# Performance work log

Measured on AMD Instinct MI355X. Metric: run time of the kernel, lower is better.

Reference implementation:

```python
import jax, jax.numpy as jnp
import numpy as np

B, S, V = 512, 256, 10      # batch, s_node_num, v_node_num
E, H = 128, 128             # embedding, lstm hidden
D = 2 * H                   # num_directions * hidden
PENALTY = 1.0e6
STD = 0.1


def _cell(x, h, c, Wih, Whh, b):
    # PyTorch LSTM cell, gate order i, f, g, o; b = b_ih + b_hh
    g = x @ Wih.T + h @ Whh.T + b
    i, f, gg, o = jnp.split(g, 4, axis=-1)
    c = jax.nn.sigmoid(f) * c + jax.nn.sigmoid(i) * jnp.tanh(gg)
    h = jax.nn.sigmoid(o) * jnp.tanh(c)
    return h, c


def setup_inputs() -> dict:
    key = jax.random.key(0)
    ks = jax.random.split(key, 25)
    w = lambda k, shp: (jax.random.normal(k, shp, jnp.float32) * STD)
    return {
        's_node_indexes': jax.random.randint(ks[0], (B, S), 0, S, dtype=jnp.int32),
        's_inputs': jax.random.uniform(ks[1], (B, S, 3), jnp.float32),
        'v_input': jax.random.uniform(ks[2], (V, 3), jnp.float32) * 0.5,
        'W_embed': w(ks[3], (E, 1)),
        'enc_Wih_f': w(ks[4], (4 * H, E)), 'enc_Whh_f': w(ks[5], (4 * H, H)), 'enc_b_f': w(ks[6], (4 * H,)),
        'enc_Wih_b': w(ks[7], (4 * H, E)), 'enc_Whh_b': w(ks[8], (4 * H, H)), 'enc_b_b': w(ks[9], (4 * H,)),
        'dec_Wih_f': w(ks[10], (4 * H, D)), 'dec_Whh_f': w(ks[11], (4 * H, H)), 'dec_b_f': w(ks[12], (4 * H,)),
        'dec_Wih_b': w(ks[13], (4 * H, D)), 'dec_Whh_b': w(ks[14], (4 * H, H)), 'dec_b_b': w(ks[15], (4 * H,)),
        'W_ref': w(ks[16], (D, D)), 'W_q': w(ks[17], (D, D)), 'v_w': w(ks[18], (D,)),
        'W_ref2': w(ks[19], (D, D)), 'W_q2': w(ks[20], (D, D)), 'v2_w': w(ks[21], (D,)),
    }


def reference(s_node_indexes, s_inputs, v_input, W_embed,
              enc_Wih_f, enc_Whh_f, enc_b_f, enc_Wih_b, enc_Whh_b, enc_b_b,
              dec_Wih_f, dec_Whh_f, dec_b_f, dec_Wih_b, dec_Whh_b, dec_b_b,
              W_ref, W_q, v_w, W_ref2, W_q2, v2_w):
    Bn, Sn = s_node_indexes.shape
    # Embed: snode resource -> Linear(1, E, bias=False)
    emb = s_inputs[:, :, 0:1] @ W_embed.T            # (B, S, E)
    xs = jnp.swapaxes(emb, 0, 1)                     # (S, B, E)
    h0 = jnp.zeros((Bn, H), jnp.float32)
    c0 = jnp.zeros((Bn, H), jnp.float32)

    def enc_scan(Wih, Whh, b, seq):
        def step(carry, x):
            h, c = carry
            h, c = _cell(x, h, c, Wih, Whh, b)
            return (h, c), h
        (hT, cT), hs = jax.lax.scan(step, (h0, c0), seq)
        return hs, hT, cT

    hs_f, hf, cf = enc_scan(enc_Wih_f, enc_Whh_f, enc_b_f, xs)
    hs_b, hb, cb = enc_scan(enc_Wih_b, enc_Whh_b, enc_b_b, xs[::-1])
    Enc = jnp.swapaxes(jnp.concatenate([hs_f, hs_b[::-1]], axis=-1), 0, 1)  # (B, S, D)
    h_state = jnp.stack([hf, hb])                    # (2, B, H)
    c_state = jnp.stack([cf, cb])

    refE = Enc @ W_ref.T                             # (B, S, D) precomputed (dropout p=0)
    ref2E = Enc @ W_ref2.T

    def dec_step(carry, vcpu):
        dec_in, h, c, played = carry                 # dec_in (B, D)
        hf_, cf_ = _cell(dec_in, h[0], c[0], dec_Wih_f, dec_Whh_f, dec_b_f)
        hb_, cb_ = _cell(dec_in, h[1], c[1], dec_Wih_b, dec_Whh_b, dec_b_b)
        dec_out = jnp.concatenate([hf_, hb_], axis=-1)                       # (B, D)
        cannot = (s_inputs[:, :, 0] < vcpu).astype(jnp.float32) + played     # (B, S)
        ow = jnp.tanh(refE + (dec_out @ W_q.T)[:, None, :]) @ v_w - PENALTY * cannot
        att = jax.nn.softmax(jnp.tanh(ref2E + (dec_in @ W_q2.T)[:, None, :]) @ v2_w, axis=1)
        new_in = jnp.einsum('bs,bsd->bd', att, Enc)
        sel = jnp.argmax(ow, axis=1)
        played = played + jax.nn.one_hot(sel, Sn, dtype=jnp.float32)
        return (new_in, jnp.stack([hf_, hb_]), jnp.stack([cf_, cb_]), played), (ow, sel)

    init = (jnp.zeros((Bn, D), jnp.float32), h_state, c_state, jnp.zeros((Bn, Sn), jnp.float32))
    _, (output_weights, sels) = jax.lax.scan(dec_step, init, v_input[:, 0])
    shuffled = sels.T                                # (B, V)
    original = jnp.take_along_axis(s_node_indexes, shuffled, axis=1)
    return original, shuffled, output_weights        # output_weights: (V, B, S)
```

## Files before the change

### kernel.cpp

```cpp
#include <hip/hip_runtime.h>
#include <math.h>

#define cB 512
#define cS 256
#define cV 10
#define cE 128
#define cH 128
#define cD 256
#define cG 512
#define PEN 1.0e6f
#define PADK 40
#define S1OW 112
#define L1OW 144
#define S2AT 128
#define L2AT 128

typedef _Float16 half8_t __attribute__((ext_vector_type(8)));
typedef _Float16 half4_t __attribute__((ext_vector_type(4)));
typedef float f32x4 __attribute__((ext_vector_type(4)));

#define DOT4(acc, wv, hv)                                   \
    do {                                                    \
        acc = fmaf((wv).x, (hv).x, acc);                    \
        acc = fmaf((wv).y, (hv).y, acc);                    \
        acc = fmaf((wv).z, (hv).z, acc);                    \
        acc = fmaf((wv).w, (hv).w, acc);                    \
    } while (0)

__device__ __forceinline__ float sigmf(float x) { return 1.0f / (1.0f + expf(-x)); }

__global__ void k_uprep(const float* __restrict__ Wih_f, const float* __restrict__ Wih_b,
                        const float* __restrict__ W_embed, float* __restrict__ uvec)
{
    const int j = threadIdx.x;
    const float* __restrict__ Wih = blockIdx.x ? Wih_b : Wih_f;
    float u = 0.f;
#pragma unroll 8
    for (int e = 0; e < cE; ++e) u = fmaf(Wih[(size_t)j * cE + e], W_embed[e], u);
    uvec[blockIdx.x * cG + j] = u;
}

__global__ __launch_bounds__(1024, 2) void k_encoder(
    const float* __restrict__ s_inputs, const float* __restrict__ uvec,
    const float* __restrict__ Whh_f, const float* __restrict__ b_f,
    const float* __restrict__ Whh_b, const float* __restrict__ b_b,
    _Float16* __restrict__ Ehi, _Float16* __restrict__ Elo,
    float* __restrict__ h_state, float* __restrict__ c_state)
{
    const int dir = blockIdx.x >> 7;
    const int b0  = (blockIdx.x & 127) * 4;
    const float* __restrict__ Whh = dir ? Whh_b : Whh_f;
    const float* __restrict__ bv  = dir ? b_b   : b_f;
    const int tid = threadIdx.x;
    const int jj = tid & 255;
    const int q  = tid >> 8;

    __shared__ __align__(16) float a_in[4][cS];
    __shared__ __align__(16) float hbuf[4][132];
    __shared__ __align__(16) float gpart[16][520];

    a_in[tid >> 8][tid & 255] =
        s_inputs[((size_t)(b0 + (tid >> 8)) * cS + (tid & 255)) * 3];

    float4 w0[8], w1[8];
#pragma unroll
    for (int kk = 0; kk < 8; ++kk) {
        w0[kk] = *(const float4*)&Whh[(size_t)jj * cH + q * 32 + kk * 4];
        w1[kk] = *(const float4*)&Whh[(size_t)(jj + 256) * cH + q * 32 + kk * 4];
    }

    const float uj0 = (q == 0) ? uvec[dir * cG + jj] : 0.f;
    const float bj0 = (q == 0) ? bv[jj] : 0.f;
    const float uj1 = (q == 0) ? uvec[dir * cG + jj + 256] : 0.f;
    const float bj1 = (q == 0) ? bv[jj + 256] : 0.f;

    const int ur = tid >> 7, uk = tid & 127;
    float c_reg = 0.f, h_last = 0.f;
    if (tid < 512) hbuf[ur][uk] = 0.f;
    __syncthreads();

    for (int p = 0; p < cS; ++p) {
        const int s = dir ? (cS - 1 - p) : p;
        float a0[4], a1[4];
#pragma unroll
        for (int r = 0; r < 4; ++r) {
            a0[r] = fmaf(a_in[r][s], uj0, bj0);
            a1[r] = fmaf(a_in[r][s], uj1, bj1);
        }
#pragma unroll
        for (int kk = 0; kk < 8; ++kk) {
            const float4 wv0 = w0[kk];
            const float4 wv1 = w1[kk];
#pragma unroll
            for (int r = 0; r < 4; ++r) {
                const float4 h4 = *(const float4*)&hbuf[r][q * 32 + kk * 4];
                DOT4(a0[r], wv0, h4);
                DOT4(a1[r], wv1, h4);
            }
        }
#pragma unroll
        for (int r = 0; r < 4; ++r) {
            gpart[r * 4 + q][jj]       = a0[r];
            gpart[r * 4 + q][jj + 256] = a1[r];
        }
        __syncthreads();

        if (tid < 512) {
            float gi = 0.f, gf = 0.f, gg = 0.f, go = 0.f;
#pragma unroll
            for (int qq = 0; qq < 4; ++qq) {
                gi += gpart[ur * 4 + qq][uk];
                gf += gpart[ur * 4 + qq][128 + uk];
                gg += gpart[ur * 4 + qq][256 + uk];
                go += gpart[ur * 4 + qq][384 + uk];
            }
            const float i_ = sigmf(gi), f_ = sigmf(gf), g_ = tanhf(gg), o_ = sigmf(go);
            c_reg = fmaf(f_, c_reg, i_ * g_);
            const float hn = o_ * tanhf(c_reg);
            h_last = hn;
            hbuf[ur][uk] = hn;
            const size_t eidx = ((size_t)(b0 + ur) * cS + s) * cD + dir * cH + uk;
            const _Float16 hh = (_Float16)hn;
            Ehi[eidx] = hh;
            Elo[eidx] = (_Float16)(hn - (float)hh);
        }
        __syncthreads();
    }
    if (tid < 512) {
        h_state[((size_t)dir * cB + b0 + ur) * cH + uk] = h_last;
        c_state[((size_t)dir * cB + b0 + ur) * cH + uk] = c_reg;
    }
}

__global__ void k_split_w(const float* __restrict__ W1, const float* __restrict__ W2,
                          _Float16* __restrict__ Whi1, _Float16* __restrict__ Wlo1,
                          _Float16* __restrict__ Whi2, _Float16* __restrict__ Wlo2)
{
    const int i = blockIdx.x * 256 + threadIdx.x;
    {
        float a = W1[i]; _Float16 h = (_Float16)a;
        Whi1[i] = h; Wlo1[i] = (_Float16)(a - (float)h);
    }
    {
        float a = W2[i]; _Float16 h = (_Float16)a;
        Whi2[i] = h; Wlo2[i] = (_Float16)(a - (float)h);
    }
}

__global__ __launch_bounds__(256) void k_head_mat2(
    const _Float16* __restrict__ Ahi, const _Float16* __restrict__ Alo,
    const _Float16* __restrict__ Whi1, const _Float16* __restrict__ Wlo1,
    const _Float16* __restrict__ Whi2, const _Float16* __restrict__ Wlo2,
    float* __restrict__ refC, float* __restrict__ ref2C)
{
    const int blk = blockIdx.x;
    const bool is1 = blk < (S1OW * cB / 64);
    const _Float16* __restrict__ Whi = is1 ? Whi1 : Whi2;
    const _Float16* __restrict__ Wlo = is1 ? Wlo1 : Wlo2;
    float* __restrict__ outv = is1 ? refC : ref2C;
    const int m0 = (is1 ? blk : blk - S1OW * cB / 64) * 64;

    const int tid = threadIdx.x;
    const int w = tid >> 6, l = tid & 63;

    __shared__ __align__(16) _Float16 As[2][64][PADK];
    __shared__ __align__(16) _Float16 Ws[2][256][PADK];

    const int r = tid >> 2, kq = tid & 3;
    size_t arow;
    {
        const int m = m0 + r;
        const int s = m >> 9, b = m & 511;
        arow = ((size_t)b * cS + s) * cD;
    }
    const size_t wrow = (size_t)tid * cD;

    f32x4 acc[16];
#pragma unroll
    for (int i = 0; i < 16; ++i) acc[i] = (f32x4){0.f, 0.f, 0.f, 0.f};

    const int fr = w * 16 + (l & 15);
    const int kc = (l >> 4) * 8;

    for (int k0 = 0; k0 < 256; k0 += 32) {
        __syncthreads();
        *(uint4*)&As[0][r][kq * 8] = *(const uint4*)&Ahi[arow + k0 + kq * 8];
        *(uint4*)&As[1][r][kq * 8] = *(const uint4*)&Alo[arow + k0 + kq * 8];
#pragma unroll
        for (int q4 = 0; q4 < 4; ++q4) {
            *(uint4*)&Ws[0][tid][q4 * 8] = *(const uint4*)&Whi[wrow + k0 + q4 * 8];
            *(uint4*)&Ws[1][tid][q4 * 8] = *(const uint4*)&Wlo[wrow + k0 + q4 * 8];
        }
        __syncthreads();

        const half8_t ahi = *(const half8_t*)&As[0][fr][kc];
        const half8_t alo = *(const half8_t*)&As[1][fr][kc];
#pragma unroll
        for (int nf = 0; nf < 16; ++nf) {
            const int n = nf * 16 + (l & 15);
            const half8_t bhi = *(const half8_t*)&Ws[0][n][kc];
            const half8_t blo = *(const half8_t*)&Ws[1][n][kc];
            acc[nf] = __builtin_amdgcn_mfma_f32_16x16x32_f16(ahi, bhi, acc[nf], 0, 0, 0);
            acc[nf] = __builtin_amdgcn_mfma_f32_16x16x32_f16(ahi, blo, acc[nf], 0, 0, 0);
            acc[nf] = __builtin_amdgcn_mfma_f32_16x16x32_f16(alo, bhi, acc[nf], 0, 0, 0);
        }
    }
#pragma unroll
    for (int nf = 0; nf < 16; ++nf)
#pragma unroll
        for (int rr = 0; rr < 4; ++rr) {
            const int m = w * 16 + ((l >> 4) << 2) + rr;
            outv[(size_t)(m0 + m) * cD + nf * 16 + (l & 15)] = acc[nf][rr];
        }
}

__global__ __launch_bounds__(512, 2) void k_score(
    const _Float16* __restrict__ Ahi, const _Float16* __restrict__ Alo,
    const _Float16* __restrict__ Whi1, const _Float16* __restrict__ Wlo1,
    const _Float16* __restrict__ Whi2, const _Float16* __restrict__ Wlo2,
    const float* __restrict__ refC, const float* __restrict__ ref2C,
    const float* __restrict__ q1v, const float* __restrict__ q2v,
    const float* __restrict__ v_w, const float* __restrict__ v2_w,
    float* __restrict__ sc1lo, float* __restrict__ sc1hi,
    float* __restrict__ sc2lo, float* __restrict__ sc2hi)
{
    __shared__ __align__(16) char smem[65536];
    const int blk = blockIdx.x;
    const int tid = threadIdx.x;

    if (blk < 1088) {
        const bool isow = blk < 576;
        const _Float16* __restrict__ Whi = isow ? Whi1 : Whi2;
        const _Float16* __restrict__ Wlo = isow ? Wlo1 : Wlo2;
        const int batt = blk - 576;
        const int m0 = isow ? blk * 128 : 0;

        _Float16 (*Ah)[PADK] = (_Float16(*)[PADK])(smem);
        _Float16 (*Al)[PADK] = (_Float16(*)[PADK])(smem + 10240);
        _Float16 (*Wh)[PADK] = (_Float16(*)[PADK])(smem + 20480);
        _Float16 (*Wl)[PADK] = (_Float16(*)[PADK])(smem + 40960);
        float* qs = (float*)(smem + 61440);
        float* vs = (float*)(smem + 62464);
        float (*spart)[128] = (float(*)[128])(smem + 63488);

        const int l = tid & 63;
        const int w = tid >> 6;
        const int wm = w >> 2, wn = w & 3;
        const int g = l >> 4, li = l & 15;

        if (isow) {
            if (tid < 256) vs[tid] = v_w[tid];
        } else {
            if (tid < 256) qs[tid] = q2v[(size_t)batt * cD + tid];
            else           vs[tid - 256] = v2_w[tid - 256];
        }

        const int ar = tid >> 2, aq = tid & 3;
        size_t arow;
        if (isow) {
            const int m = m0 + ar;
            const int bq = m / L1OW;
            const int s = S1OW + (m - bq * L1OW);
            arow = ((size_t)bq * cS + s) * cD;
        } else {
            arow = ((size_t)batt * cS + S2AT + ar) * cD;
        }

        f32x4 acc[4][4];
#pragma unroll
        for (int mi = 0; mi < 4; ++mi)
#pragma unroll
            for (int ni = 0; ni < 4; ++ni) acc[mi][ni] = (f32x4){0.f, 0.f, 0.f, 0.f};

        for (int k0 = 0; k0 < 256; k0 += 32) {
            __syncthreads();
            *(uint4*)&Ah[ar][aq * 8] = *(const uint4*)&Ahi[arow + k0 + aq * 8];
            *(uint4*)&Al[ar][aq * 8] = *(const uint4*)&Alo[arow + k0 + aq * 8];
            *(uint4*)&Wh[ar][aq * 8] = *(const uint4*)&Whi[(size_t)ar * cD + k0 + aq * 8];
            *(uint4*)&Wl[ar][aq * 8] = *(const uint4*)&Wlo[(size_t)ar * cD + k0 + aq * 8];
            *(uint4*)&Wh[ar + 128][aq * 8] = *(const uint4*)&Whi[(size_t)(ar + 128) * cD + k0 + aq * 8];
            *(uint4*)&Wl[ar + 128][aq * 8] = *(const uint4*)&Wlo[(size_t)(ar + 128) * cD + k0 + aq * 8];
            __syncthreads();

            half8_t ah[4], al[4];
#pragma unroll
            for (int mi = 0; mi < 4; ++mi) {
                ah[mi] = *(const half8_t*)&Ah[wm * 64 + mi * 16 + li][g * 8];
                al[mi] = *(const half8_t*)&Al[wm * 64 + mi * 16 + li][g * 8];
            }
#pragma unroll
            for (int ni = 0; ni < 4; ++ni) {
                const half8_t bh = *(const half8_t*)&Wh[wn * 64 + ni * 16 + li][g * 8];
                const half8_t bl = *(const half8_t*)&Wl[wn * 64 + ni * 16 + li][g * 8];
#pragma unroll
                for (int mi = 0; mi < 4; ++mi) {
                    acc[mi][ni] = __builtin_amdgcn_mfma_f32_16x16x32_f16(ah[mi], bh, acc[mi][ni], 0, 0, 0);
                    acc[mi][ni] = __builtin_amdgcn_mfma_f32_16x16x32_f16(ah[mi], bl, acc[mi][ni], 0, 0, 0);
                    acc[mi][ni] = __builtin_amdgcn_mfma_f32_16x16x32_f16(al[mi], bh, acc[mi][ni], 0, 0, 0);
                }
            }
        }

        float val = 0.f;
#pragma unroll
        for (int mi = 0; mi < 4; ++mi)
#pragma unroll
            for (int rr = 0; rr < 4; ++rr) {
                const int row = wm * 64 + mi * 16 + g * 4 + rr;
                float p = 0.f;
#pragma unroll
                for (int ni = 0; ni < 4; ++ni) {
                    const int c = wn * 64 + ni * 16 + li;
                    const float qq = isow ? q1v[(size_t)((m0 + row) / L1OW) * cD + c]
                                          : qs[c];
                    p = fmaf(vs[c], tanhf(acc[mi][ni][rr] + qq), p);
                }
                p += __shfl_xor(p, 1);
                p += __shfl_xor(p, 2);
                p += __shfl_xor(p, 4);
                p += __shfl_xor(p, 8);
                if (li == mi * 4 + rr) val = p;
            }
        {
            const int row_out = wm * 64 + (li >> 2) * 16 + g * 4 + (li & 3);
            spart[wn][row_out] = val;
        }
        __syncthreads();
        if (tid < 128) {
            const float o = spart[0][tid] + spart[1][tid] + spart[2][tid] + spart[3][tid];
            if (isow) sc1hi[m0 + tid] = o;
            else      sc2hi[(size_t)batt * L2AT + tid] = o;
        }
    } else {
        const int fb = blk - 1088;
        const bool isowf = fb < 448;
        const float* __restrict__ C  = isowf ? refC : ref2C;
        const float* __restrict__ qv = isowf ? q1v : q2v;
        const float* __restrict__ vv = isowf ? v_w : v2_w;
        float* __restrict__ outv     = isowf ? sc1lo : sc2lo;
        const int m0 = (isowf ? fb : fb - 448) * 128;

        float (*red)[4] = (float(*)[4])smem;
        const int r = tid >> 2, p2 = tid & 3;
        const int m = m0 + r;
        const int b = m & 511;

        const float* row  = C + (size_t)m * cD + p2 * 64;
        const float* qrow = qv + (size_t)b * cD + p2 * 64;
        const float* vrow = vv + p2 * 64;
        float s = 0.f;
#pragma unroll 4
        for (int d = 0; d < 64; d += 4) {
            const float4 rv4 = *(const float4*)&row[d];
            const float4 q4  = *(const float4*)&qrow[d];
            const float4 v4  = *(const float4*)&vrow[d];
            s = fmaf(v4.x, tanhf(rv4.x + q4.x), s);
            s = fmaf(v4.y, tanhf(rv4.y + q4.y), s);
            s = fmaf(v4.z, tanhf(rv4.z + q4.z), s);
            s = fmaf(v4.w, tanhf(rv4.w + q4.w), s);
        }
        red[r][p2] = s;
        __syncthreads();
        if (tid < 128)
            outv[m0 + tid] = red[tid][0] + red[tid][1] + red[tid][2] + red[tid][3];
    }
}

__global__ __launch_bounds__(512, 2) void k_dec_cells(
    const float* __restrict__ dec_in,
    const float* __restrict__ Wih_f, const float* __restrict__ Whh_f, const float* __restrict__ b_f,
    const float* __restrict__ Wih_b, const float* __restrict__ Whh_b, const float* __restrict__ b_b,
    float* __restrict__ h_state, float* __restrict__ c_state, float* __restrict__ dec_out)
{
    const int cell = blockIdx.x >> 7;
    const int b0 = (blockIdx.x & 127) * 4;
    const float* __restrict__ Wih = cell ? Wih_b : Wih_f;
    const float* __restrict__ Whh = cell ? Whh_b : Whh_f;
    const float* __restrict__ bv  = cell ? b_b   : b_f;
    const int j = threadIdx.x;

    __shared__ __align__(16) float xin[4][cD];
    __shared__ __align__(16) float hin[4][cH];
    __shared__ __align__(16) float gbuf[4][cG];

    for (int idx = j; idx < 4 * cD; idx += 512) {
        int bb = idx >> 8, k = idx & 255;
        xin[bb][k] = dec_in[(size_t)(b0 + bb) * cD + k];
    }
    {
        int bb = j >> 7, k = j & 127;
        hin[bb][k] = h_state[((size_t)cell * cB + b0 + bb) * cH + k];
    }
    __syncthreads();

    float a0 = bv[j];
    float a1 = a0, a2 = a0, a3 = a0;
#pragma unroll 4
    for (int kk = 0; kk < 64; ++kk) {
        const float4 wv = *(const float4*)&Wih[(size_t)j * cD + kk * 4];
        const float4 x0 = *(const float4*)&xin[0][kk * 4]; DOT4(a0, wv, x0);
        const float4 x1 = *(const float4*)&xin[1][kk * 4]; DOT4(a1, wv, x1);
        const float4 x2 = *(const float4*)&xin[2][kk * 4]; DOT4(a2, wv, x2);
        const float4 x3 = *(const float4*)&xin[3][kk * 4]; DOT4(a3, wv, x3);
    }
#pragma unroll 4
    for (int kk = 0; kk < 32; ++kk) {
        const float4 wv = *(const float4*)&Whh[(size_t)j * cH + kk * 4];
        const float4 h0 = *(const float4*)&hin[0][kk * 4]; DOT4(a0, wv, h0);
        const float4 h1 = *(const float4*)&hin[1][kk * 4]; DOT4(a1, wv, h1);
        const float4 h2 = *(const float4*)&hin[2][kk * 4]; DOT4(a2, wv, h2);
        const float4 h3 = *(const float4*)&hin[3][kk * 4]; DOT4(a3, wv, h3);
    }
    gbuf[0][j] = a0; gbuf[1][j] = a1; gbuf[2][j] = a2; gbuf[3][j] = a3;
    __syncthreads();

    const int uk = j & 127, ub = j >> 7;
    const float gi = gbuf[ub][uk];
    const float gf = gbuf[ub][128 + uk];
    const float gg = gbuf[ub][256 + uk];
    const float go = gbuf[ub][384 + uk];
    const size_t sidx = ((size_t)cell * cB + b0 + ub) * cH + uk;
    const float c_old = c_state[sidx];
    const float i_ = sigmf(gi), f_ = sigmf(gf), g_ = tanhf(gg), o_ = sigmf(go);
    const float cn = fmaf(f_, c_old, i_ * g_);
    const float hn = o_ * tanhf(cn);
    c_state[sidx] = cn;
    h_state[sidx] = hn;
    dec_out[(size_t)(b0 + ub) * cD + cell * cH + uk] = hn;
}

__global__ __launch_bounds__(256, 2) void k_qproj(
    const float* __restrict__ dec_out, const float* __restrict__ dec_in_old,
    const float* __restrict__ W_q, const float* __restrict__ W_q2,
    float* __restrict__ q1v, float* __restrict__ q2v)
{
    const int b = blockIdx.x;
    const int tid = threadIdx.x;
    __shared__ __align__(16) float dout[cD];
    __shared__ __align__(16) float din[cD];
    dout[tid] = dec_out[(size_t)b * cD + tid];
    din[tid]  = dec_in_old[(size_t)b * cD + tid];
    __syncthreads();
    float s1 = 0.0f, s2 = 0.0f;
#pragma unroll 4
    for (int kk = 0; kk < 64; ++kk) {
        const float4 w1 = *(const float4*)&W_q[(size_t)tid * cD + kk * 4];
        const float4 w2 = *(const float4*)&W_q2[(size_t)tid * cD + kk * 4];
        const float4 x1 = *(const float4*)&dout[kk * 4];
        const float4 x2 = *(const float4*)&din[kk * 4];
        DOT4(s1, w1, x1);
        DOT4(s2, w2, x2);
    }
    q1v[(size_t)b * cD + tid] = s1;
    q2v[(size_t)b * cD + tid] = s2;
}

__global__ __launch_bounds__(256, 2) void k_finish(
    const float* __restrict__ sc1lo, const float* __restrict__ sc1hi,
    const float* __restrict__ sc2lo, const float* __restrict__ sc2hi,
    const _Float16* __restrict__ Ehi, const _Float16* __restrict__ Elo,
    const float* __restrict__ s_inputs, const int* __restrict__ s_node_indexes,
    const float* __restrict__ v_input, float* __restrict__ played,
    float* __restrict__ dec_in_new, float* __restrict__ outp, int t)
{
    const int b = blockIdx.x;
    const int tid = threadIdx.x;
    const int lane = tid & 63;
    const int wv = tid >> 6;

    __shared__ __align__(16) float atr[cS];
    __shared__ __align__(16) float part[4][cD];
    __shared__ float rv[cS];
    __shared__ int   ri[cS];

    const float owv = (tid < S1OW) ? sc1lo[(size_t)tid * cB + b]
                                   : sc1hi[(size_t)b * L1OW + (tid - S1OW)];
    atr[tid] = (tid < S2AT) ? sc2lo[(size_t)tid * cB + b]
                            : sc2hi[(size_t)b * L2AT + (tid - S2AT)];

    const float vcpu = v_input[t * 3];
    float val;
    {
        const float a0 = s_inputs[((size_t)b * cS + tid) * 3];
        const float can = (a0 < vcpu ? 1.0f : 0.0f) + played[(size_t)b * cS + tid];
        val = owv - PEN * can;
        outp[2 * cB * cV + ((size_t)t * cB + b) * cS + tid] = val;
    }
    rv[tid] = val; ri[tid] = tid;
    __syncthreads();
#pragma unroll
    for (int off = 128; off > 0; off >>= 1) {
        if (tid < off) {
            const float v2 = rv[tid + off]; const int i2 = ri[tid + off];
            const float v1 = rv[tid];       const int i1 = ri[tid];
            if (v2 > v1 || (v2 == v1 && i2 < i1)) { rv[tid] = v2; ri[tid] = i2; }
        }
        __syncthreads();
    }
    const int sel = ri[0];
    __syncthreads();
    if (tid == 0) {
        played[(size_t)b * cS + sel] += 1.0f;
        outp[(size_t)b * cV + t] = (float)s_node_indexes[(size_t)b * cS + sel];
        outp[(size_t)cB * cV + (size_t)b * cV + t] = (float)sel;
    }

    rv[tid] = atr[tid];
    __syncthreads();
#pragma unroll
    for (int off = 128; off > 0; off >>= 1) {
        if (tid < off) { const float v2 = rv[tid + off]; if (v2 > rv[tid]) rv[tid] = v2; }
        __syncthreads();
    }
    const float mx = rv[0];
    __syncthreads();
    const float ex = expf(atr[tid] - mx);
    rv[tid] = ex;
    __syncthreads();
#pragma unroll
    for (int off = 128; off > 0; off >>= 1) {
        if (tid < off) rv[tid] += rv[tid + off];
        __syncthreads();
    }
    const float ssum = rv[0];
    __syncthreads();
    atr[tid] = ex / ssum;
    __syncthreads();

    {
        float4 acc = make_float4(0.f, 0.f, 0.f, 0.f);
        for (int s2i = wv * 64; s2i < wv * 64 + 64; ++s2i) {
            const float a = atr[s2i];
            const size_t eidx = ((size_t)b * cS + s2i) * cD + lane * 4;
            const half4_t h4 = *(const half4_t*)&Ehi[eidx];
            const half4_t l4 = *(const half4_t*)&Elo[eidx];
            acc.x = fmaf(a, (float)h4[0] + (float)l4[0], acc.x);
            acc.y = fmaf(a, (float)h4[1] + (float)l4[1], acc.y);
            acc.z = fmaf(a, (float)h4[2] + (float)l4[2], acc.z);
            acc.w = fmaf(a, (float)h4[3] + (float)l4[3], acc.w);
        }
        *(float4*)&part[wv][lane * 4] = acc;
    }
    __syncthreads();
    dec_in_new[(size_t)b * cD + tid] =
        part[0][tid] + part[1][tid] + part[2][tid] + part[3][tid];
}

extern "C" void kernel_launch(void* const* d_in, const int* in_sizes, int n_in,
                              void* d_out, int out_size, void* d_ws, size_t ws_size,
                              hipStream_t stream)
{
    (void)in_sizes; (void)n_in; (void)out_size; (void)ws_size;

    const int*   s_node = (const int*)  d_in[0];
    const float* s_inp  = (const float*)d_in[1];
    const float* v_inp  = (const float*)d_in[2];
    const float* W_emb  = (const float*)d_in[3];
    const float* eWih_f = (const float*)d_in[4];
    const float* eWhh_f = (const float*)d_in[5];
    const float* eb_f   = (const float*)d_in[6];
    const float* eWih_b = (const float*)d_in[7];
    const float* eWhh_b = (const float*)d_in[8];
    const float* eb_b   = (const float*)d_in[9];
    const float* dWih_f = (const float*)d_in[10];
    const float* dWhh_f = (const float*)d_in[11];
    const float* db_f   = (const float*)d_in[12];
    const float* dWih_b = (const float*)d_in[13];
    const float* dWhh_b = (const float*)d_in[14];
    const float* db_b   = (const float*)d_in[15];
    const float* W_ref  = (const float*)d_in[16];
    const float* W_q    = (const float*)d_in[17];
    const float* v_w    = (const float*)d_in[18];
    const float* W_ref2 = (const float*)d_in[19];
    const float* W_q2   = (const float*)d_in[20];
    const float* v2_w   = (const float*)d_in[21];

    float* out = (float*)d_out;
    const size_t ENCSZ = (size_t)cB * cS * cD;
    const size_t SMALL = (size_t)cB * cD;

    char* p = (char*)d_ws;
    _Float16* Ehi  = (_Float16*)p; p += ENCSZ * 2;
    _Float16* Elo  = (_Float16*)p; p += ENCSZ * 2;
    float* refC    = (float*)p;    p += (size_t)S1OW * cB * cD * 4;
    float* ref2C   = (float*)p;    p += (size_t)S2AT * cB * cD * 4;
    _Float16* Whi1 = (_Float16*)p; p += (size_t)cD * cD * 2;
    _Float16* Wlo1 = (_Float16*)p; p += (size_t)cD * cD * 2;
    _Float16* Whi2 = (_Float16*)p; p += (size_t)cD * cD * 2;
    _Float16* Wlo2 = (_Float16*)p; p += (size_t)cD * cD * 2;
    float* hst    = (float*)p; p += SMALL * 4;
    float* cst    = (float*)p; p += SMALL * 4;
    float* din0   = (float*)p; p += SMALL * 4;
    float* din1   = (float*)p; p += SMALL * 4;
    float* doutb  = (float*)p; p += SMALL * 4;
    float* played = (float*)p; p += SMALL * 4;
    float* q1v    = (float*)p; p += SMALL * 4;
    float* q2v    = (float*)p; p += SMALL * 4;
    float* sc1lo  = (float*)p; p += (size_t)S1OW * cB * 4;
    float* sc1hi  = (float*)p; p += (size_t)L1OW * cB * 4;
    float* sc2lo  = (float*)p; p += (size_t)S2AT * cB * 4;
    float* sc2hi  = (float*)p; p += (size_t)L2AT * cB * 4;
    float* uvec   = (float*)p; p += 2 * cG * 4;

    hipMemsetAsync(played, 0, SMALL * sizeof(float), stream);
    hipMemsetAsync(din0,   0, SMALL * sizeof(float), stream);

    k_split_w<<<256, 256, 0, stream>>>(W_ref, W_ref2, Whi1, Wlo1, Whi2, Wlo2);
    k_uprep<<<2, 512, 0, stream>>>(eWih_f, eWih_b, W_emb, uvec);

    k_encoder<<<256, 1024, 0, stream>>>(s_inp, uvec, eWhh_f, eb_f, eWhh_b, eb_b,
                                        Ehi, Elo, hst, cst);

    k_head_mat2<<<(S1OW + S2AT) * cB / 64, 256, 0, stream>>>(
        Ehi, Elo, Whi1, Wlo1, Whi2, Wlo2, refC, ref2C);

    for (int t = 0; t < cV; ++t) {
        float* di_old = (t & 1) ? din1 : din0;
        float* di_new = (t & 1) ? din0 : din1;
        k_dec_cells<<<256, 512, 0, stream>>>(di_old, dWih_f, dWhh_f, db_f,
                                             dWih_b, dWhh_b, db_b, hst, cst, doutb);
        k_qproj<<<512, 256, 0, stream>>>(doutb, di_old, W_q, W_q2, q1v, q2v);
        k_score<<<2048, 512, 0, stream>>>(Ehi, Elo, Whi1, Wlo1, Whi2, Wlo2,
                                          refC, ref2C, q1v, q2v, v_w, v2_w,
                                          sc1lo, sc1hi, sc2lo, sc2hi);
        k_finish<<<512, 256, 0, stream>>>(sc1lo, sc1hi, sc2lo, sc2hi, Ehi, Elo,
                                          s_inp, s_node, v_inp, played, di_new, out, t);
    }
}
```

Baseline: 2.996 ms.

## Fuse per-step decoder kernels into one persistent cooperative kernel with grid syncs

The four per-timestep decoder kernels (LSTM cells, query projection, scoring, finish) are turned into device functions. A single cooperative kernel loops over all ten steps, with each phase separated by grid.sync(), which replaces 40 separate launches. Blocks stride over the logical block indices of each phase. The point is to remove launch gaps and per-launch overhead. In exchange, every phase now runs with 512-thread blocks, so the half-idle 256-thread phases waste lanes. It also adds grid-wide barrier cost and relies on co-residency of the chosen grid size, with a non-cooperative fallback path if the cooperative launch fails.

Result: slower. 3.624 ms (+21.0%).

```diff
diff --git a/kernel.cpp b/kernel.cpp
--- a/kernel.cpp
+++ b/kernel.cpp
@@ -1,5 +1,8 @@
 #include <hip/hip_runtime.h>
+#include <hip/hip_cooperative_groups.h>
 #include <math.h>
+
+namespace cg = cooperative_groups;
 
 #define cB 512
 #define cS 256
@@ -214,24 +217,118 @@
         }
 }
 
-__global__ __launch_bounds__(512, 2) void k_score(
-    const _Float16* __restrict__ Ahi, const _Float16* __restrict__ Alo,
-    const _Float16* __restrict__ Whi1, const _Float16* __restrict__ Wlo1,
-    const _Float16* __restrict__ Whi2, const _Float16* __restrict__ Wlo2,
-    const float* __restrict__ refC, const float* __restrict__ ref2C,
-    const float* __restrict__ q1v, const float* __restrict__ q2v,
-    const float* __restrict__ v_w, const float* __restrict__ v2_w,
-    float* __restrict__ sc1lo, float* __restrict__ sc1hi,
-    float* __restrict__ sc2lo, float* __restrict__ sc2hi)
-{
-    __shared__ __align__(16) char smem[65536];
-    const int blk = blockIdx.x;
+struct DecArgs {
+    const _Float16 *Ehi, *Elo;
+    const _Float16 *Whi1, *Wlo1, *Whi2, *Wlo2;
+    const float *refC, *ref2C;
+    float *q1v, *q2v;
+    const float *v_w, *v2_w;
+    float *sc1lo, *sc1hi, *sc2lo, *sc2hi;
+    const float *dWih_f, *dWhh_f, *db_f, *dWih_b, *dWhh_b, *db_b;
+    float *hst, *cst, *din0, *din1, *doutb, *played;
+    const float *s_inp;
+    const int *s_node;
+    const float *v_inp;
+    const float *W_q, *W_q2;
+    float *out;
+};
+
+__device__ void cells_phase(const DecArgs& a, char* smem, int lb, const float* dec_in)
+{
+    const int cell = lb >> 7;
+    const int b0 = (lb & 127) * 4;
+    const float* __restrict__ Wih = cell ? a.dWih_b : a.dWih_f;
+    const float* __restrict__ Whh = cell ? a.dWhh_b : a.dWhh_f;
+    const float* __restrict__ bv  = cell ? a.db_b   : a.db_f;
+    const int j = threadIdx.x;
+
+    float (*xin)[cD]  = (float(*)[cD])(smem);
+    float (*hin)[cH]  = (float(*)[cH])(smem + 4096);
+    float (*gbuf)[cG] = (float(*)[cG])(smem + 6144);
+
+    for (int idx = j; idx < 4 * cD; idx += 512) {
+        int bb = idx >> 8, k = idx & 255;
+        xin[bb][k] = dec_in[(size_t)(b0 + bb) * cD + k];
+    }
+    {
+        int bb = j >> 7, k = j & 127;
+        hin[bb][k] = a.hst[((size_t)cell * cB + b0 + bb) * cH + k];
+    }
+    __syncthreads();
+
+    float a0 = bv[j];
+    float a1 = a0, a2 = a0, a3 = a0;
+#pragma unroll 4
+    for (int kk = 0; kk < 64; ++kk) {
+        const float4 wv = *(const float4*)&Wih[(size_t)j * cD + kk * 4];
+        const float4 x0 = *(const float4*)&xin[0][kk * 4]; DOT4(a0, wv, x0);
+        const float4 x1 = *(const float4*)&xin[1][kk * 4]; DOT4(a1, wv, x1);
+        const float4 x2 = *(const float4*)&xin[2][kk * 4]; DOT4(a2, wv, x2);
+        const float4 x3 = *(const float4*)&xin[3][kk * 4]; DOT4(a3, wv, x3);
+    }
+#pragma unroll 4
+    for (int kk = 0; kk < 32; ++kk) {
+        const float4 wv = *(const float4*)&Whh[(size_t)j * cH + kk * 4];
+        const float4 h0 = *(const float4*)&hin[0][kk * 4]; DOT4(a0, wv, h0);
+        const float4 h1 = *(const float4*)&hin[1][kk * 4]; DOT4(a1, wv, h1);
+        const float4 h2 = *(const float4*)&hin[2][kk * 4]; DOT4(a2, wv, h2);
+        const float4 h3 = *(const float4*)&hin[3][kk * 4]; DOT4(a3, wv, h3);
+    }
+    gbuf[0][j] = a0; gbuf[1][j] = a1; gbuf[2][j] = a2; gbuf[3][j] = a3;
+    __syncthreads();
+
+    const int uk = j & 127, ub = j >> 7;
+    const float gi = gbuf[ub][uk];
+    const float gf = gbuf[ub][128 + uk];
+    const float gg = gbuf[ub][256 + uk];
+    const float go = gbuf[ub][384 + uk];
+    const size_t sidx = ((size_t)cell * cB + b0 + ub) * cH + uk;
+    const float c_old = a.cst[sidx];
+    const float i_ = sigmf(gi), f_ = sigmf(gf), g_ = tanhf(gg), o_ = sigmf(go);
+    const float cn = fmaf(f_, c_old, i_ * g_);
+    const float hn = o_ * tanhf(cn);
+    a.cst[sidx] = cn;
+    a.hst[sidx] = hn;
+    a.doutb[(size_t)(b0 + ub) * cD + cell * cH + uk] = hn;
+    __syncthreads();
+}
+
+__device__ void qproj_phase(const DecArgs& a, char* smem, int b, const float* dec_in_old)
+{
     const int tid = threadIdx.x;
+    float* dout = (float*)smem;
+    float* din  = (float*)(smem + 1024);
+    if (tid < 256) {
+        dout[tid] = a.doutb[(size_t)b * cD + tid];
+        din[tid]  = dec_in_old[(size_t)b * cD + tid];
+    }
+    __syncthreads();
+    if (tid < 256) {
+        float s1 = 0.0f, s2 = 0.0f;
+#pragma unroll 4
+        for (int kk = 0; kk < 64; ++kk) {
+            const float4 w1 = *(const float4*)&a.W_q[(size_t)tid * cD + kk * 4];
+            const float4 w2 = *(const float4*)&a.W_q2[(size_t)tid * cD + kk * 4];
+            const float4 x1 = *(const float4*)&dout[kk * 4];
+            const float4 x2 = *(const float4*)&din[kk * 4];
+            DOT4(s1, w1, x1);
+            DOT4(s2, w2, x2);
+        }
+        a.q1v[(size_t)b * cD + tid] = s1;
+        a.q2v[(size_t)b * cD + tid] = s2;
+    }
+    __syncthreads();
+}
+
+__device__ void score_phase(const DecArgs& a, char* smem, int blk)
+{
+    const int tid = threadIdx.x;
+    __syncthreads();
 
     if (blk < 1088) {
         const bool isow = blk < 576;
-        const _Float16* __restrict__ Whi = isow ? Whi1 : Whi2;
-        const _Float16* __restrict__ Wlo = isow ? Wlo1 : Wlo2;
+        const _Float16* __restrict__ Whi = isow ? a.Whi1 : a.Whi2;
+        const _Float16* __restrict__ Wlo = isow ? a.Wlo1 : a.Wlo2;
         const int batt = blk - 576;
         const int m0 = isow ? blk * 128 : 0;
 
@@ -249,10 +346,10 @@
         const int g = l >> 4, li = l & 15;
 
         if (isow) {
-            if (tid < 256) vs[tid] = v_w[tid];
+            if (tid < 256) vs[tid] = a.v_w[tid];
         } else {
-            if (tid < 256) qs[tid] = q2v[(size_t)batt * cD + tid];
-            else           vs[tid - 256] = v2_w[tid - 256];
+            if (tid < 256) qs[tid] = a.q2v[(size_t)batt * cD + tid];
+            else           vs[tid - 256] = a.v2_w[tid - 256];
         }
 
         const int ar = tid >> 2, aq = tid & 3;
@@ -274,8 +371,8 @@
 
         for (int k0 = 0; k0 < 256; k0 += 32) {
             __syncthreads();
-            *(uint4*)&Ah[ar][aq * 8] = *(const uint4*)&Ahi[arow + k0 + aq * 8];
-            *(uint4*)&Al[ar][aq * 8] = *(const uint4*)&Alo[arow + k0 + aq * 8];
+            *(uint4*)&Ah[ar][aq * 8] = *(const uint4*)&a.Ehi[arow + k0 + aq * 8];
+            *(uint4*)&Al[ar][aq * 8] = *(const uint4*)&a.Elo[arow + k0 + aq * 8];
             *(uint4*)&Wh[ar][aq * 8] = *(const uint4*)&Whi[(size_t)ar * cD + k0 + aq * 8];
             *(uint4*)&Wl[ar][aq * 8] = *(const uint4*)&Wlo[(size_t)ar * cD + k0 + aq * 8];
             *(uint4*)&Wh[ar + 128][aq * 8] = *(const uint4*)&Whi[(size_t)(ar + 128) * cD + k0 + aq * 8];
@@ -311,7 +408,7 @@
 #pragma unroll
                 for (int ni = 0; ni < 4; ++ni) {
                     const int c = wn * 64 + ni * 16 + li;
-                    const float qq = isow ? q1v[(size_t)((m0 + row) / L1OW) * cD + c]
+                    const float qq = isow ? a.q1v[(size_t)((m0 + row) / L1OW) * cD + c]
                                           : qs[c];
                     p = fmaf(vs[c], tanhf(acc[mi][ni][rr] + qq), p);
                 }
@@ -328,16 +425,16 @@
         __syncthreads();
         if (tid < 128) {
             const float o = spart[0][tid] + spart[1][tid] + spart[2][tid] + spart[3][tid];
-            if (isow) sc1hi[m0 + tid] = o;
-            else      sc2hi[(size_t)batt * L2AT + tid] = o;
+            if (isow) a.sc1hi[m0 + tid] = o;
+            else      a.sc2hi[(size_t)batt * L2AT + tid] = o;
         }
     } else {
         const int fb = blk - 1088;
         const bool isowf = fb < 448;
-        const float* __restrict__ C  = isowf ? refC : ref2C;
-        const float* __restrict__ qv = isowf ? q1v : q2v;
-        const float* __restrict__ vv = isowf ? v_w : v2_w;
-        float* __restrict__ outv     = isowf ? sc1lo : sc2lo;
+        const float* __restrict__ C  = isowf ? a.refC : a.ref2C;
+        const float* __restrict__ qv = isowf ? a.q1v : a.q2v;
+        const float* __restrict__ vv = isowf ? a.v_w : a.v2_w;
+        float* __restrict__ outv     = isowf ? a.sc1lo : a.sc2lo;
         const int m0 = (isowf ? fb : fb - 448) * 128;
 
         float (*red)[4] = (float(*)[4])smem;
@@ -366,127 +463,31 @@
     }
 }
 
-__global__ __launch_bounds__(512, 2) void k_dec_cells(
-    const float* __restrict__ dec_in,
-    const float* __restrict__ Wih_f, const float* __restrict__ Whh_f, const float* __restrict__ b_f,
-    const float* __restrict__ Wih_b, const float* __restrict__ Whh_b, const float* __restrict__ b_b,
-    float* __restrict__ h_state, float* __restrict__ c_state, float* __restrict__ dec_out)
-{
-    const int cell = blockIdx.x >> 7;
-    const int b0 = (blockIdx.x & 127) * 4;
-    const float* __restrict__ Wih = cell ? Wih_b : Wih_f;
-    const float* __restrict__ Whh = cell ? Whh_b : Whh_f;
-    const float* __restrict__ bv  = cell ? b_b   : b_f;
-    const int j = threadIdx.x;
-
-    __shared__ __align__(16) float xin[4][cD];
-    __shared__ __align__(16) float hin[4][cH];
-    __shared__ __align__(16) float gbuf[4][cG];
-
-    for (int idx = j; idx < 4 * cD; idx += 512) {
-        int bb = idx >> 8, k = idx & 255;
-        xin[bb][k] = dec_in[(size_t)(b0 + bb) * cD + k];
-    }
-    {
-        int bb = j >> 7, k = j & 127;
-        hin[bb][k] = h_state[((size_t)cell * cB + b0 + bb) * cH + k];
-    }
-    __syncthreads();
-
-    float a0 = bv[j];
-    float a1 = a0, a2 = a0, a3 = a0;
-#pragma unroll 4
-    for (int kk = 0; kk < 64; ++kk) {
-        const float4 wv = *(const float4*)&Wih[(size_t)j * cD + kk * 4];
-        const float4 x0 = *(const float4*)&xin[0][kk * 4]; DOT4(a0, wv, x0);
-        const float4 x1 = *(const float4*)&xin[1][kk * 4]; DOT4(a1, wv, x1);
-        const float4 x2 = *(const float4*)&xin[2][kk * 4]; DOT4(a2, wv, x2);
-        const float4 x3 = *(const float4*)&xin[3][kk * 4]; DOT4(a3, wv, x3);
-    }
-#pragma unroll 4
-    for (int kk = 0; kk < 32; ++kk) {
-        const float4 wv = *(const float4*)&Whh[(size_t)j * cH + kk * 4];
-        const float4 h0 = *(const float4*)&hin[0][kk * 4]; DOT4(a0, wv, h0);
-        const float4 h1 = *(const float4*)&hin[1][kk * 4]; DOT4(a1, wv, h1);
-        const float4 h2 = *(const float4*)&hin[2][kk * 4]; DOT4(a2, wv, h2);
-        const float4 h3 = *(const float4*)&hin[3][kk * 4]; DOT4(a3, wv, h3);
-    }
-    gbuf[0][j] = a0; gbuf[1][j] = a1; gbuf[2][j] = a2; gbuf[3][j] = a3;
-    __syncthreads();
-
-    const int uk = j & 127, ub = j >> 7;
-    const float gi = gbuf[ub][uk];
-    const float gf = gbuf[ub][128 + uk];
-    const float gg = gbuf[ub][256 + uk];
-    const float go = gbuf[ub][384 + uk];
-    const size_t sidx = ((size_t)cell * cB + b0 + ub) * cH + uk;
-    const float c_old = c_state[sidx];
-    const float i_ = sigmf(gi), f_ = sigmf(gf), g_ = tanhf(gg), o_ = sigmf(go);
-    const float cn = fmaf(f_, c_old, i_ * g_);
-    const float hn = o_ * tanhf(cn);
-    c_state[sidx] = cn;
-    h_state[sidx] = hn;
-    dec_out[(size_t)(b0 + ub) * cD + cell * cH + uk] = hn;
-}
-
-__global__ __launch_bounds__(256, 2) void k_qproj(
-    const float* __restrict__ dec_out, const float* __restrict__ dec_in_old,
-    const float* __restrict__ W_q, const float* __restrict__ W_q2,
-    float* __restrict__ q1v, float* __restrict__ q2v)
-{
-    const int b = blockIdx.x;
-    const int tid = threadIdx.x;
-    __shared__ __align__(16) float dout[cD];
-    __shared__ __align__(16) float din[cD];
-    dout[tid] = dec_out[(size_t)b * cD + tid];
-    din[tid]  = dec_in_old[(size_t)b * cD + tid];
-    __syncthreads();
-    float s1 = 0.0f, s2 = 0.0f;
-#pragma unroll 4
-    for (int kk = 0; kk < 64; ++kk) {
-        const float4 w1 = *(const float4*)&W_q[(size_t)tid * cD + kk * 4];
-        const float4 w2 = *(const float4*)&W_q2[(size_t)tid * cD + kk * 4];
-        const float4 x1 = *(const float4*)&dout[kk * 4];
-        const float4 x2 = *(const float4*)&din[kk * 4];
-        DOT4(s1, w1, x1);
-        DOT4(s2, w2, x2);
-    }
-    q1v[(size_t)b * cD + tid] = s1;
-    q2v[(size_t)b * cD + tid] = s2;
-}
-
-__global__ __launch_bounds__(256, 2) void k_finish(
-    const float* __restrict__ sc1lo, const float* __restrict__ sc1hi,
-    const float* __restrict__ sc2lo, const float* __restrict__ sc2hi,
-    const _Float16* __restrict__ Ehi, const _Float16* __restrict__ Elo,
-    const float* __restrict__ s_inputs, const int* __restrict__ s_node_indexes,
-    const float* __restrict__ v_input, float* __restrict__ played,
-    float* __restrict__ dec_in_new, float* __restrict__ outp, int t)
-{
-    const int b = blockIdx.x;
+__device__ void finish_phase(const DecArgs& a, char* smem, int b, int t, float* dec_in_new)
+{
     const int tid = threadIdx.x;
     const int lane = tid & 63;
     const int wv = tid >> 6;
 
-    __shared__ __align__(16) float atr[cS];
-    __shared__ __align__(16) float part[4][cD];
-    __shared__ float rv[cS];
-    __shared__ int   ri[cS];
-
-    const float owv = (tid < S1OW) ? sc1lo[(size_t)tid * cB + b]
-                                   : sc1hi[(size_t)b * L1OW + (tid - S1OW)];
-    atr[tid] = (tid < S2AT) ? sc2lo[(size_t)tid * cB + b]
-                            : sc2hi[(size_t)b * L2AT + (tid - S2AT)];
-
-    const float vcpu = v_input[t * 3];
-    float val;
-    {
-        const float a0 = s_inputs[((size_t)b * cS + tid) * 3];
-        const float can = (a0 < vcpu ? 1.0f : 0.0f) + played[(size_t)b * cS + tid];
-        val = owv - PEN * can;
-        outp[2 * cB * cV + ((size_t)t * cB + b) * cS + tid] = val;
-    }
-    rv[tid] = val; ri[tid] = tid;
+    float* atr = (float*)smem;
+    float (*part)[cD] = (float(*)[cD])(smem + 1024);
+    float* rv = (float*)(smem + 5120);
+    int*   ri = (int*)(smem + 6144);
+
+    float ex = 0.f;
+    if (tid < 256) {
+        const float owv = (tid < S1OW) ? a.sc1lo[(size_t)tid * cB + b]
+                                       : a.sc1hi[(size_t)b * L1OW + (tid - S1OW)];
+        atr[tid] = (tid < S2AT) ? a.sc2lo[(size_t)tid * cB + b]
+                                : a.sc2hi[(size_t)b * L2AT + (tid - S2AT)];
+
+        const float vcpu = a.v_inp[t * 3];
+        const float a0 = a.s_inp[((size_t)b * cS + tid) * 3];
+        const float can = (a0 < vcpu ? 1.0f : 0.0f) + a.played[(size_t)b * cS + tid];
+        const float val = owv - PEN * can;
+        a.out[2 * cB * cV + ((size_t)t * cB + b) * cS + tid] = val;
+        rv[tid] = val; ri[tid] = tid;
+    }
     __syncthreads();
 #pragma unroll
     for (int off = 128; off > 0; off >>= 1) {
@@ -500,12 +501,12 @@
     const int sel = ri[0];
     __syncthreads();
     if (tid == 0) {
-        played[(size_t)b * cS + sel] += 1.0f;
-        outp[(size_t)b * cV + t] = (float)s_node_indexes[(size_t)b * cS + sel];
-        outp[(size_t)cB * cV + (size_t)b * cV + t] = (float)sel;
-    }
-
-    rv[tid] = atr[tid];
+        a.played[(size_t)b * cS + sel] += 1.0f;
+        a.out[(size_t)b * cV + t] = (float)a.s_node[(size_t)b * cS + sel];
+        a.out[(size_t)cB * cV + (size_t)b * cV + t] = (float)sel;
+    }
+
+    if (tid < 256) rv[tid] = atr[tid];
     __syncthreads();
 #pragma unroll
     for (int off = 128; off > 0; off >>= 1) {
@@ -514,8 +515,10 @@
     }
     const float mx = rv[0];
     __syncthreads();
-    const float ex = expf(atr[tid] - mx);
-    rv[tid] = ex;
+    if (tid < 256) {
+        ex = expf(atr[tid] - mx);
+        rv[tid] = ex;
+    }
     __syncthreads();
 #pragma unroll
     for (int off = 128; off > 0; off >>= 1) {
@@ -524,26 +527,77 @@
     }
     const float ssum = rv[0];
     __syncthreads();
-    atr[tid] = ex / ssum;
-    __syncthreads();
-
-    {
+    if (tid < 256) atr[tid] = ex / ssum;
+    __syncthreads();
+
+    if (tid < 256) {
         float4 acc = make_float4(0.f, 0.f, 0.f, 0.f);
         for (int s2i = wv * 64; s2i < wv * 64 + 64; ++s2i) {
-            const float a = atr[s2i];
+            const float aw = atr[s2i];
             const size_t eidx = ((size_t)b * cS + s2i) * cD + lane * 4;
-            const half4_t h4 = *(const half4_t*)&Ehi[eidx];
-            const half4_t l4 = *(const half4_t*)&Elo[eidx];
-            acc.x = fmaf(a, (float)h4[0] + (float)l4[0], acc.x);
-            acc.y = fmaf(a, (float)h4[1] + (float)l4[1], acc.y);
-            acc.z = fmaf(a, (float)h4[2] + (float)l4[2], acc.z);
-            acc.w = fmaf(a, (float)h4[3] + (float)l4[3], acc.w);
+            const half4_t h4 = *(const half4_t*)&a.Ehi[eidx];
+            const half4_t l4 = *(const half4_t*)&a.Elo[eidx];
+            acc.x = fmaf(aw, (float)h4[0] + (float)l4[0], acc.x);
+            acc.y = fmaf(aw, (float)h4[1] + (float)l4[1], acc.y);
+            acc.z = fmaf(aw, (float)h4[2] + (float)l4[2], acc.z);
+            acc.w = fmaf(aw, (float)h4[3] + (float)l4[3], acc.w);
         }
         *(float4*)&part[wv][lane * 4] = acc;
     }
     __syncthreads();
-    dec_in_new[(size_t)b * cD + tid] =
-        part[0][tid] + part[1][tid] + part[2][tid] + part[3][tid];
+    if (tid < 256)
+        dec_in_new[(size_t)b * cD + tid] =
+            part[0][tid] + part[1][tid] + part[2][tid] + part[3][tid];
+    __syncthreads();
+}
+
+__global__ __launch_bounds__(512, 2) void k_decode(DecArgs a)
+{
+    __shared__ __align__(16) char smem[65536];
+    cg::grid_group grid = cg::this_grid();
+    const int nb = (int)gridDim.x;
+
+    for (int t = 0; t < cV; ++t) {
+        float* di_old = (t & 1) ? a.din1 : a.din0;
+        float* di_new = (t & 1) ? a.din0 : a.din1;
+
+        for (int lb = (int)blockIdx.x; lb < 256; lb += nb)
+            cells_phase(a, smem, lb, di_old);
+        __threadfence(); grid.sync();
+
+        for (int lb = (int)blockIdx.x; lb < 512; lb += nb)
+            qproj_phase(a, smem, lb, di_old);
+        __threadfence(); grid.sync();
+
+        for (int lb = (int)blockIdx.x; lb < 2048; lb += nb)
+            score_phase(a, smem, lb);
+        __threadfence(); grid.sync();
+
+        for (int lb = (int)blockIdx.x; lb < 512; lb += nb)
+            finish_phase(a, smem, lb, t, di_new);
+        __threadfence(); grid.sync();
+    }
+}
+
+__global__ __launch_bounds__(512, 2) void k_cells_fb(DecArgs a, const float* di_old)
+{
+    __shared__ __align__(16) char smem[16384];
+    cells_phase(a, smem, (int)blockIdx.x, di_old);
+}
+__global__ __launch_bounds__(512, 2) void k_qproj_fb(DecArgs a, const float* di_old)
+{
+    __shared__ __align__(16) char smem[4096];
+    qproj_phase(a, smem, (int)blockIdx.x, di_old);
+}
+__global__ __launch_bounds__(512, 2) void k_score_fb(DecArgs a)
+{
+    __shared__ __align__(16) char smem[65536];
+    score_phase(a, smem, (int)blockIdx.x);
+}
+__global__ __launch_bounds__(512, 2) void k_finish_fb(DecArgs a, int t, float* di_new)
+{
+    __shared__ __align__(16) char smem[8192];
+    finish_phase(a, smem, (int)blockIdx.x, t, di_new);
 }
 
 extern "C" void kernel_launch(void* const* d_in, const int* in_sizes, int n_in,
@@ -614,16 +668,44 @@
     k_head_mat2<<<(S1OW + S2AT) * cB / 64, 256, 0, stream>>>(
         Ehi, Elo, Whi1, Wlo1, Whi2, Wlo2, refC, ref2C);
 
-    for (int t = 0; t < cV; ++t) {
-        float* di_old = (t & 1) ? din1 : din0;
-        float* di_new = (t & 1) ? din0 : din1;
-        k_dec_cells<<<256, 512, 0, stream>>>(di_old, dWih_f, dWhh_f, db_f,
-                                             dWih_b, dWhh_b, db_b, hst, cst, doutb);
-        k_qproj<<<512, 256, 0, stream>>>(doutb, di_old, W_q, W_q2, q1v, q2v);
-        k_score<<<2048, 512, 0, stream>>>(Ehi, Elo, Whi1, Wlo1, Whi2, Wlo2,
-                                          refC, ref2C, q1v, q2v, v_w, v2_w,
-                                          sc1lo, sc1hi, sc2lo, sc2hi);
-        k_finish<<<512, 256, 0, stream>>>(sc1lo, sc1hi, sc2lo, sc2hi, Ehi, Elo,
-                                          s_inp, s_node, v_inp, played, di_new, out, t);
-    }
-}
+    DecArgs da;
+    da.Ehi = Ehi; da.Elo = Elo;
+    da.Whi1 = Whi1; da.Wlo1 = Wlo1; da.Whi2 = Whi2; da.Wlo2 = Wlo2;
+    da.refC = refC; da.ref2C = ref2C;
+    da.q1v = q1v; da.q2v = q2v;
+    da.v_w = v_w; da.v2_w = v2_w;
+    da.sc1lo = sc1lo; da.sc1hi = sc1hi; da.sc2lo = sc2lo; da.sc2hi = sc2hi;
+    da.dWih_f = dWih_f; da.dWhh_f = dWhh_f; da.db_f = db_f;
+    da.dWih_b = dWih_b; da.dWhh_b = dWhh_b; da.db_b = db_b;
+    da.hst = hst; da.cst = cst; da.din0 = din0; da.din1 = din1;
+    da.doutb = doutb; da.played = played;
+    da.s_inp = s_inp; da.s_node = s_node; da.v_inp = v_inp;
+    da.W_q = W_q; da.W_q2 = W_q2;
+    da.out = out;
+
+    int coop = 0, dev = 0;
+    hipGetDevice(&dev);
+    hipDeviceGetAttribute(&coop, hipDeviceAttributeCooperativeLaunch, dev);
+    int nbper = 0;
+    hipOccupancyMaxActiveBlocksPerMultiprocessor(&nbper, (const void*)k_decode, 512, 0);
+
+    bool did_coop = false;
+    if (coop && nbper >= 1) {
+        const int grid = (nbper >= 2) ? 512 : 256;
+        void* kargs[] = { &da };
+        if (hipLaunchCooperativeKernel((const void*)k_decode, dim3(grid), dim3(512),
+                                       kargs, 0, stream) == hipSuccess)
+            did_coop = true;
+    }
+
+    if (!did_coop) {
+        for (int t = 0; t < cV; ++t) {
+            float* di_old = (t & 1) ? din1 : din0;
+            float* di_new = (t & 1) ? din0 : din1;
+            k_cells_fb<<<256, 512, 0, stream>>>(da, di_old);
+            k_qproj_fb<<<512, 512, 0, stream>>>(da, di_old);
+            k_score_fb<<<2048, 512, 0, stream>>>(da);
+            k_finish_fb<<<512, 512, 0, stream>>>(da, t, di_new);
+        }
+    }
+}
```

## Fuse decoder LSTM cells and query projection into one kernel

Applied to the files above, without the earlier changes.

Merges the per-step decoder LSTM cell kernel and the W_q/W_q2 query projection kernel into a single 1024-thread kernel that handles both directions for 4 batch rows, passing the new hidden state to the projection through shared memory. This removes one launch per decode step and a global round trip of dec_out and dec_in. In exchange the grid shrinks to 128 blocks of 1024 threads, which may lower occupancy, and the projection now reads W_q rows once per 4 batch rows rather than once per row.

New measurement: 3.468 ms. 1.16x slower.

```diff
diff --git a/kernel.cpp b/kernel.cpp
--- a/kernel.cpp
+++ b/kernel.cpp
@@ -366,30 +366,35 @@
     }
 }
 
-__global__ __launch_bounds__(512, 2) void k_dec_cells(
+__global__ __launch_bounds__(1024, 4) void k_cells_qp(
     const float* __restrict__ dec_in,
     const float* __restrict__ Wih_f, const float* __restrict__ Whh_f, const float* __restrict__ b_f,
     const float* __restrict__ Wih_b, const float* __restrict__ Whh_b, const float* __restrict__ b_b,
-    float* __restrict__ h_state, float* __restrict__ c_state, float* __restrict__ dec_out)
-{
-    const int cell = blockIdx.x >> 7;
-    const int b0 = (blockIdx.x & 127) * 4;
+    const float* __restrict__ W_q, const float* __restrict__ W_q2,
+    float* __restrict__ h_state, float* __restrict__ c_state, float* __restrict__ dec_out,
+    float* __restrict__ q1v, float* __restrict__ q2v)
+{
+    const int b0 = blockIdx.x * 4;
+    const int tid = threadIdx.x;
+    const int cell = tid >> 9;
+    const int j = tid & 511;
+
     const float* __restrict__ Wih = cell ? Wih_b : Wih_f;
     const float* __restrict__ Whh = cell ? Whh_b : Whh_f;
     const float* __restrict__ bv  = cell ? b_b   : b_f;
-    const int j = threadIdx.x;
 
     __shared__ __align__(16) float xin[4][cD];
-    __shared__ __align__(16) float hin[4][cH];
-    __shared__ __align__(16) float gbuf[4][cG];
-
-    for (int idx = j; idx < 4 * cD; idx += 512) {
-        int bb = idx >> 8, k = idx & 255;
-        xin[bb][k] = dec_in[(size_t)(b0 + bb) * cD + k];
-    }
-    {
-        int bb = j >> 7, k = j & 127;
-        hin[bb][k] = h_state[((size_t)cell * cB + b0 + bb) * cH + k];
+    __shared__ __align__(16) float hin[2][4][cH];
+    __shared__ __align__(16) float gbuf[2][4][cG];
+    __shared__ __align__(16) float dout[4][cD];
+
+    {
+        const int bb = tid >> 8, k = tid & 255;
+        if (tid < 1024) xin[bb & 3][k] = dec_in[(size_t)(b0 + (bb & 3)) * cD + k];
+    }
+    {
+        const int c2 = tid >> 9, bb = (tid >> 7) & 3, k = tid & 127;
+        hin[c2][bb][k] = h_state[((size_t)c2 * cB + b0 + bb) * cH + k];
     }
     __syncthreads();
 
@@ -406,53 +411,48 @@
 #pragma unroll 4
     for (int kk = 0; kk < 32; ++kk) {
         const float4 wv = *(const float4*)&Whh[(size_t)j * cH + kk * 4];
-        const float4 h0 = *(const float4*)&hin[0][kk * 4]; DOT4(a0, wv, h0);
-        const float4 h1 = *(const float4*)&hin[1][kk * 4]; DOT4(a1, wv, h1);
-        const float4 h2 = *(const float4*)&hin[2][kk * 4]; DOT4(a2, wv, h2);
-        const float4 h3 = *(const float4*)&hin[3][kk * 4]; DOT4(a3, wv, h3);
-    }
-    gbuf[0][j] = a0; gbuf[1][j] = a1; gbuf[2][j] = a2; gbuf[3][j] = a3;
-    __syncthreads();
-
-    const int uk = j & 127, ub = j >> 7;
-    const float gi = gbuf[ub][uk];
-    const float gf = gbuf[ub][128 + uk];
-    const float gg = gbuf[ub][256 + uk];
-    const float go = gbuf[ub][384 + uk];
-    const size_t sidx = ((size_t)cell * cB + b0 + ub) * cH + uk;
-    const float c_old = c_state[sidx];
-    const float i_ = sigmf(gi), f_ = sigmf(gf), g_ = tanhf(gg), o_ = sigmf(go);
-    const float cn = fmaf(f_, c_old, i_ * g_);
-    const float hn = o_ * tanhf(cn);
-    c_state[sidx] = cn;
-    h_state[sidx] = hn;
-    dec_out[(size_t)(b0 + ub) * cD + cell * cH + uk] = hn;
-}
-
-__global__ __launch_bounds__(256, 2) void k_qproj(
-    const float* __restrict__ dec_out, const float* __restrict__ dec_in_old,
-    const float* __restrict__ W_q, const float* __restrict__ W_q2,
-    float* __restrict__ q1v, float* __restrict__ q2v)
-{
-    const int b = blockIdx.x;
-    const int tid = threadIdx.x;
-    __shared__ __align__(16) float dout[cD];
-    __shared__ __align__(16) float din[cD];
-    dout[tid] = dec_out[(size_t)b * cD + tid];
-    din[tid]  = dec_in_old[(size_t)b * cD + tid];
-    __syncthreads();
-    float s1 = 0.0f, s2 = 0.0f;
+        const float4 h0 = *(const float4*)&hin[cell][0][kk * 4]; DOT4(a0, wv, h0);
+        const float4 h1 = *(const float4*)&hin[cell][1][kk * 4]; DOT4(a1, wv, h1);
+        const float4 h2 = *(const float4*)&hin[cell][2][kk * 4]; DOT4(a2, wv, h2);
+        const float4 h3 = *(const float4*)&hin[cell][3][kk * 4]; DOT4(a3, wv, h3);
+    }
+    gbuf[cell][0][j] = a0; gbuf[cell][1][j] = a1;
+    gbuf[cell][2][j] = a2; gbuf[cell][3][j] = a3;
+    __syncthreads();
+
+    {
+        const int c2 = tid >> 9, ub = (tid >> 7) & 3, uk = tid & 127;
+        const float gi = gbuf[c2][ub][uk];
+        const float gf = gbuf[c2][ub][128 + uk];
+        const float gg = gbuf[c2][ub][256 + uk];
+        const float go = gbuf[c2][ub][384 + uk];
+        const size_t sidx = ((size_t)c2 * cB + b0 + ub) * cH + uk;
+        const float c_old = c_state[sidx];
+        const float i_ = sigmf(gi), f_ = sigmf(gf), g_ = tanhf(gg), o_ = sigmf(go);
+        const float cn = fmaf(f_, c_old, i_ * g_);
+        const float hn = o_ * tanhf(cn);
+        c_state[sidx] = cn;
+        h_state[sidx] = hn;
+        dec_out[(size_t)(b0 + ub) * cD + c2 * cH + uk] = hn;
+        dout[ub][c2 * cH + uk] = hn;
+    }
+    __syncthreads();
+
+    {
+        const int bb = tid >> 8, d = tid & 255;
+        float s1 = 0.0f, s2 = 0.0f;
 #pragma unroll 4
-    for (int kk = 0; kk < 64; ++kk) {
-        const float4 w1 = *(const float4*)&W_q[(size_t)tid * cD + kk * 4];
-        const float4 w2 = *(const float4*)&W_q2[(size_t)tid * cD + kk * 4];
-        const float4 x1 = *(const float4*)&dout[kk * 4];
-        const float4 x2 = *(const float4*)&din[kk * 4];
-        DOT4(s1, w1, x1);
-        DOT4(s2, w2, x2);
-    }
-    q1v[(size_t)b * cD + tid] = s1;
-    q2v[(size_t)b * cD + tid] = s2;
+        for (int kk = 0; kk < 64; ++kk) {
+            const float4 w1 = *(const float4*)&W_q[(size_t)d * cD + kk * 4];
+            const float4 w2 = *(const float4*)&W_q2[(size_t)d * cD + kk * 4];
+            const float4 x1 = *(const float4*)&dout[bb][kk * 4];
+            const float4 x2 = *(const float4*)&xin[bb][kk * 4];
+            DOT4(s1, w1, x1);
+            DOT4(s2, w2, x2);
+        }
+        q1v[(size_t)(b0 + bb) * cD + d] = s1;
+        q2v[(size_t)(b0 + bb) * cD + d] = s2;
+    }
 }
 
 __global__ __launch_bounds__(256, 2) void k_finish(
@@ -617,9 +617,9 @@
     for (int t = 0; t < cV; ++t) {
         float* di_old = (t & 1) ? din1 : din0;
         float* di_new = (t & 1) ? din0 : din1;
-        k_dec_cells<<<256, 512, 0, stream>>>(di_old, dWih_f, dWhh_f, db_f,
-                                             dWih_b, dWhh_b, db_b, hst, cst, doutb);
-        k_qproj<<<512, 256, 0, stream>>>(doutb, di_old, W_q, W_q2, q1v, q2v);
+        k_cells_qp<<<128, 1024, 0, stream>>>(di_old, dWih_f, dWhh_f, db_f,
+                                             dWih_b, dWhh_b, db_b, W_q, W_q2,
+                                             hst, cst, doutb, q1v, q2v);
         k_score<<<2048, 512, 0, stream>>>(Ehi, Elo, Whi1, Wlo1, Whi2, Wlo2,
                                           refC, ref2C, q1v, q2v, v_w, v2_w,
                                           sc1lo, sc1hi, sc2lo, sc2hi);
```
